# Kernel optimization log

Hardware: AMD Instinct MI355X
Metric: run time of the kernel (lower is better)

## Reference

```python
import jax, jax.numpy as jnp
import numpy as np

N = 100000   # nodes
E = 800000   # directed edges (symmetrized to 2E in forward)
D0 = 128     # input feature dim (dim0)
H = 128      # hidden = h_dim * args.d = 64 * 2
L = 4        # num_layers
G = 64       # num graphs for global_mean_pool
BN_EPS = 1e-5
LN_EPS = 1e-5


def setup_inputs() -> dict:
    key = jax.random.key(0)
    ks = jax.random.split(key, 12)
    s = 1.0 / np.sqrt(H)
    x = jax.random.normal(ks[0], (N, D0), dtype=jnp.float32)
    row = jax.random.randint(ks[1], (E,), 0, N, dtype=jnp.int32)
    off = jax.random.randint(ks[2], (E,), 1, N, dtype=jnp.int32)
    col = (row + off) % N  # guarantees row != col (no self loops)
    edge_index = jnp.stack([row, col])
    batch = jnp.sort(jax.random.randint(ks[3], (N,), 0, G, dtype=jnp.int32))
    return {
        "x": x,
        "W0": jax.random.normal(ks[4], (D0, H), dtype=jnp.float32) * s,
        "b0": jnp.zeros((H,), jnp.float32),
        "eps_l": jnp.zeros((L,), jnp.float32),        # GIN eps per layer
        "W1": jax.random.normal(ks[5], (L, H, H), dtype=jnp.float32) * s,
        "b1": jnp.zeros((L, H), jnp.float32),
        "bn_g": jnp.ones((L, H), jnp.float32),
        "bn_b": jnp.zeros((L, H), jnp.float32),
        "W2": jax.random.normal(ks[6], (L, H, H), dtype=jnp.float32) * s,
        "b2": jnp.zeros((L, H), jnp.float32),
        "ln_g": jnp.ones((L, H), jnp.float32),
        "ln_b": jnp.zeros((L, H), jnp.float32),
        "edge_index": edge_index,
        "batch": batch,
    }


def reference(x, W0, b0, eps_l, W1, b1, bn_g, bn_b, W2, b2, ln_g, ln_b, edge_index, batch):
    n = x.shape[0]
    h = x @ W0 + b0  # layer0 encode -> [N, H]
    # FNSD: symmetrize edges (cat with flip) and drop self loops
    ei = jnp.concatenate([edge_index, edge_index[::-1]], axis=1)
    row, col = ei[0], ei[1]
    w = (row != col).astype(h.dtype)  # self-loop removal as zero edge weight
    for i in range(L):
        # GINConv: scatter-add of neighbor features
        agg = jax.ops.segment_sum(w[:, None] * h[col], row, num_segments=n)
        u = (1.0 + eps_l[i]) * h + agg
        # mlp: Linear -> BatchNorm1d (training-mode batch stats) -> ReLU -> Linear
        z = u @ W1[i] + b1[i]
        m = jnp.mean(z, axis=0)
        v = jnp.var(z, axis=0)
        z = (z - m) * jax.lax.rsqrt(v + BN_EPS) * bn_g[i] + bn_b[i]
        z = jax.nn.relu(z)
        z = z @ W2[i] + b2[i]
        z = jax.nn.relu(z)          # use_activation
        h = h + z                    # use_residual
        mu = jnp.mean(h, axis=-1, keepdims=True)   # LayerNorm
        var = jnp.var(h, axis=-1, keepdims=True)
        h = (h - mu) * jax.lax.rsqrt(var + LN_EPS) * ln_g[i] + ln_b[i]
    # global_mean_pool over graph ids
    cnt = jax.ops.segment_sum(jnp.ones((n,), h.dtype), batch, num_segments=G)
    sums = jax.ops.segment_sum(h, batch, num_segments=G)
    return sums / jnp.maximum(cnt, 1.0)[:, None]
```

## Files before the change

kernel.cpp:

```cpp
#include <hip/hip_runtime.h>

#define NN 100000
#define EE 800000
#define HH 128
#define LL 4
#define GG 64
#define BN_EPS 1e-5f
#define LN_EPS 1e-5f
#define POOL_CHUNK 64
#define NBUK ((NN + 255) >> 8)
#define CAP 8192
#define BCHUNK 8192

typedef __attribute__((ext_vector_type(8))) short short8;
typedef __attribute__((ext_vector_type(4))) float f32x4;

__device__ inline unsigned short bf16_rne(float f) {
    unsigned u = __float_as_uint(f);
    return (unsigned short)((u + 0x7FFF + ((u >> 16) & 1)) >> 16);
}
__device__ inline float bf16_to_f32(unsigned short h) {
    return __uint_as_float((unsigned)h << 16);
}


__global__ void setup_kernel(const float* __restrict__ W0, const float* __restrict__ W1,
                             const float* __restrict__ W2, short* __restrict__ wt_hi,
                             int* __restrict__ bcur, float* __restrict__ colsum,
                             float* __restrict__ psum, float* __restrict__ pcnt) {
    int i = blockIdx.x * 256 + threadIdx.x;
    if (i < NBUK) bcur[i] = i * CAP;
    if (i < LL * HH * 2) colsum[i] = 0.f;
    if (i < GG * HH) psum[i] = 0.f;
    if (i < GG) pcnt[i] = 0.f;
    if (i < 9 * HH * HH) {
        int mat = i >> 14, rem = i & 16383;
        int n = rem >> 7, k = rem & 127;
        const float* src = (mat == 0) ? W0 : ((mat <= 4) ? W1 + (size_t)(mat - 1) * HH * HH
                                                         : W2 + (size_t)(mat - 5) * HH * HH);
        float v = src[(size_t)k * HH + n];
        int off = (mat << 14) + (((k >> 3) * 8 + (n >> 4)) << 7) + ((n & 15) << 3) + (k & 7);
        wt_hi[off] = (short)bf16_rne(v);
    }
}


__global__ __launch_bounds__(256) void bucket_scatter(const int* __restrict__ ei, int* __restrict__ bcur,
                                                      int* __restrict__ pairs) {
    __shared__ int h[NBUK];
    __shared__ int curb[NBUK];
    int tid = threadIdx.x;
    for (int i = tid; i < NBUK; i += 256) h[i] = 0;
    __syncthreads();
    int base = blockIdx.x * BCHUNK;
#pragma unroll 4
    for (int k = 0; k < BCHUNK / 256; k++) {
        int e = base + k * 256 + tid;
        if (e < 2 * EE) {
            int r = ei[e];
            int c = (e < EE) ? ei[e + EE] : ei[e - EE];
            if (r != c) atomicAdd(&h[r >> 8], 1);
        }
    }
    __syncthreads();
    for (int i = tid; i < NBUK; i += 256) {
        int n = h[i];
        curb[i] = n ? atomicAdd(&bcur[i], n) : 0;
    }
    __syncthreads();
#pragma unroll 4
    for (int k = 0; k < BCHUNK / 256; k++) {
        int e = base + k * 256 + tid;
        if (e < 2 * EE) {
            int r = ei[e];
            int c = (e < EE) ? ei[e + EE] : ei[e - EE];
            if (r != c) {
                int p = atomicAdd(&curb[r >> 8], 1);
                pairs[p] = ((r & 255) << 17) | c;
            }
        }
    }
}

__global__ __launch_bounds__(256) void bucket_build(const int* __restrict__ pairs, const int* __restrict__ bcur,
                                                    int* __restrict__ rp, int* __restrict__ re,
                                                    int* __restrict__ colidx) {
    __shared__ int hist[256], off[256], lcol[CAP];
    int b = blockIdx.x, tid = threadIdx.x;
    int s = b * CAP;
    int size = bcur[b] - s;
    hist[tid] = 0;
    __syncthreads();
    for (int i = tid; i < size; i += 256) atomicAdd(&hist[pairs[s + i] >> 17], 1);
    __syncthreads();
    off[tid] = hist[tid];
    __syncthreads();
    for (int o = 1; o < 256; o <<= 1) {
        int x = (tid >= o) ? off[tid - o] : 0;
        __syncthreads();
        off[tid] += x;
        __syncthreads();
    }
    int excl = (tid > 0) ? off[tid - 1] : 0;
    int r = (b << 8) + tid;
    if (r < NN) { rp[r] = s + excl; re[r] = s + off[tid]; }
    hist[tid] = excl;
    __syncthreads();
    for (int i = tid; i < size; i += 256) {
        int u = pairs[s + i];
        int p = atomicAdd(&hist[u >> 17], 1);
        lcol[p] = u & 0x1FFFF;
    }
    __syncthreads();
    for (int i = tid; i < size; i += 256) colidx[s + i] = lcol[i];
}


__global__ __launch_bounds__(256) void agg_kernel(
    const uint2* __restrict__ hbf2, const int* __restrict__ rp, const int* __restrict__ re,
    const int* __restrict__ colidx,
    const float* __restrict__ eps_l, int layer, uint2* __restrict__ u2)
{
    int lane = threadIdx.x & 63;
    int half = lane >> 5, sub = lane & 31;
    int node = blockIdx.x * 8 + (threadIdx.x >> 6) * 2 + half;
    float eps1 = 1.0f + eps_l[layer];
    uint2 sv = hbf2[(size_t)node * 32 + sub];
    float a0 = bf16_to_f32((unsigned short)(sv.x & 0xFFFF)) * eps1;
    float a1 = bf16_to_f32((unsigned short)(sv.x >> 16)) * eps1;
    float a2 = bf16_to_f32((unsigned short)(sv.y & 0xFFFF)) * eps1;
    float a3 = bf16_to_f32((unsigned short)(sv.y >> 16)) * eps1;
    int base = rp[node];
    int n = re[node] - base;
    for (int i = 0; i < n; i += 8) {
        uint2 v[8];
        int c[8];
#pragma unroll
        for (int j = 0; j < 8; j++) c[j] = (i + j < n) ? colidx[base + i + j] : -1;
#pragma unroll
        for (int j = 0; j < 8; j++)
            v[j] = (c[j] >= 0) ? hbf2[(size_t)c[j] * 32 + sub] : make_uint2(0u, 0u);
#pragma unroll
        for (int j = 0; j < 8; j++) {
            a0 += bf16_to_f32((unsigned short)(v[j].x & 0xFFFF));
            a1 += bf16_to_f32((unsigned short)(v[j].x >> 16));
            a2 += bf16_to_f32((unsigned short)(v[j].y & 0xFFFF));
            a3 += bf16_to_f32((unsigned short)(v[j].y >> 16));
        }
    }
    uint2 o;
    o.x = (unsigned)bf16_rne(a0) | ((unsigned)bf16_rne(a1) << 16);
    o.y = (unsigned)bf16_rne(a2) | ((unsigned)bf16_rne(a3) << 16);
    u2[(size_t)node * 32 + sub] = o;
}


template<int MODE>
__global__ __launch_bounds__(256, 4) void gemm_v9(
    const void* __restrict__ Ain,
    const short* __restrict__ wt_hi,
    const float* __restrict__ bias,
    unsigned short* __restrict__ z1_out,
    float* __restrict__ colsum, float* __restrict__ colsq,
    const float* __restrict__ bng, const float* __restrict__ bnb,
    const float* __restrict__ lng, const float* __restrict__ lnb,
    unsigned short* __restrict__ hbf)
{
    __shared__ short wh[HH * HH];
    __shared__ float stats[2 * HH];
    int tid = threadIdx.x;
    int wave = tid >> 6, lane = tid & 63;
    int lrow = lane & 15, kgrp = lane >> 4;
    int r0 = blockIdx.x * 64;
    int arow = r0 + wave * 16 + lrow;

    {
        const short8* src = (const short8*)wt_hi;
        short8* dst = (short8*)wh;
#pragma unroll
        for (int i = 0; i < 8; i++) dst[tid + i * 256] = src[tid + i * 256];
    }
    if (MODE == 1) stats[tid] = 0.f;
    if (MODE == 2 && tid < HH) {
        float m = colsum[tid] * (1.f / NN);
        float v = colsq[tid] * (1.f / NN) - m * m;
        float a = bng[tid] * rsqrtf(v + BN_EPS);
        stats[tid] = a;
        stats[HH + tid] = bnb[tid] - m * a;
    }

    float4 a0[4], a1[4];
    short8 az[4];
    if (MODE != 0) {
        const unsigned short* Az = (const unsigned short*)Ain;
        if (arow < NN) {
#pragma unroll
            for (int ks = 0; ks < 4; ks++)
                az[ks] = *(const short8*)(Az + (size_t)arow * HH + ks * 32 + kgrp * 8);
        } else {
#pragma unroll
            for (int ks = 0; ks < 4; ks++) az[ks] = (short8){0,0,0,0,0,0,0,0};
        }
    } else {
        const float* Af = (const float*)Ain;
        if (arow < NN) {
#pragma unroll
            for (int ks = 0; ks < 4; ks++) {
                int kb = ks * 32 + kgrp * 8;
                a0[ks] = *(const float4*)(Af + (size_t)arow * HH + kb);
                a1[ks] = *(const float4*)(Af + (size_t)arow * HH + kb + 4);
            }
        } else {
#pragma unroll
            for (int ks = 0; ks < 4; ks++) {
                a0[ks] = make_float4(0.f, 0.f, 0.f, 0.f);
                a1[ks] = a0[ks];
            }
        }
    }
    __syncthreads();

    f32x4 acc[8];
#pragma unroll
    for (int c = 0; c < 8; c++) acc[c] = (f32x4){0.f, 0.f, 0.f, 0.f};

#pragma unroll
    for (int ks = 0; ks < 4; ks++) {
        int fb = (ks * 4 + kgrp) * 8;
        if (MODE == 1) {
#pragma unroll
            for (int c = 0; c < 8; c++) {
                short8 whi = *(const short8*)(wh + ((fb + c) << 7) + (lrow << 3));
                acc[c] = __builtin_amdgcn_mfma_f32_16x16x32_bf16(az[ks], whi, acc[c], 0, 0, 0);
            }
        } else {
            int kb = ks * 32 + kgrp * 8;
            float av[8];
            if (MODE == 2) {
#pragma unroll
                for (int j = 0; j < 8; j++) {
                    float zb = bf16_to_f32((unsigned short)az[ks][j]);
                    av[j] = fmaxf(fmaf(zb, stats[kb + j], stats[HH + kb + j]), 0.f);
                }
            } else {
                av[0] = a0[ks].x; av[1] = a0[ks].y; av[2] = a0[ks].z; av[3] = a0[ks].w;
                av[4] = a1[ks].x; av[5] = a1[ks].y; av[6] = a1[ks].z; av[7] = a1[ks].w;
            }
            short8 ahi, alo;
#pragma unroll
            for (int j = 0; j < 8; j++) {
                unsigned short hb = bf16_rne(av[j]);
                ahi[j] = (short)hb;
                alo[j] = (short)bf16_rne(av[j] - bf16_to_f32(hb));
            }
#pragma unroll
            for (int c = 0; c < 8; c++) {
                short8 whi = *(const short8*)(wh + ((fb + c) << 7) + (lrow << 3));
                acc[c] = __builtin_amdgcn_mfma_f32_16x16x32_bf16(ahi, whi, acc[c], 0, 0, 0);
                acc[c] = __builtin_amdgcn_mfma_f32_16x16x32_bf16(alo, whi, acc[c], 0, 0, 0);
            }
        }
    }

    float bv[8];
#pragma unroll
    for (int c = 0; c < 8; c++) bv[c] = bias[c * 16 + lrow];
    int lrb = wave * 16 + kgrp * 4;
    unsigned short* hst = (unsigned short*)wh;

    if (MODE == 0) {
        __syncthreads();
#pragma unroll
        for (int c = 0; c < 8; c++)
#pragma unroll
            for (int reg = 0; reg < 4; reg++)
                hst[(lrb + reg) * HH + c * 16 + lrow] = bf16_rne(acc[c][reg] + bv[c]);
        __syncthreads();
#pragma unroll
        for (int i = 0; i < 4; i++) {
            int idx = tid + i * 256;
            int r = r0 + (idx >> 4);
            if (r < NN)
                *(uint4*)(hbf + (size_t)r * HH + (idx & 15) * 8) = ((const uint4*)wh)[idx];
        }
    } else if (MODE == 1) {
        __syncthreads();
        float ps[8], pq[8];
#pragma unroll
        for (int c = 0; c < 8; c++) { ps[c] = 0.f; pq[c] = 0.f; }
#pragma unroll
        for (int c = 0; c < 8; c++)
#pragma unroll
            for (int reg = 0; reg < 4; reg++) {
                float z = acc[c][reg] + bv[c];
                hst[(lrb + reg) * HH + c * 16 + lrow] = bf16_rne(z);
                if (r0 + lrb + reg < NN) { ps[c] += z; pq[c] += z * z; }
            }
#pragma unroll
        for (int c = 0; c < 8; c++) {
            ps[c] += __shfl_xor(ps[c], 16); pq[c] += __shfl_xor(pq[c], 16);
            ps[c] += __shfl_xor(ps[c], 32); pq[c] += __shfl_xor(pq[c], 32);
        }
        if (kgrp == 0) {
#pragma unroll
            for (int c = 0; c < 8; c++) {
                atomicAdd(&stats[c * 16 + lrow], ps[c]);
                atomicAdd(&stats[HH + c * 16 + lrow], pq[c]);
            }
        }
        __syncthreads();
#pragma unroll
        for (int i = 0; i < 4; i++) {
            int idx = tid + i * 256;
            int r = r0 + (idx >> 4);
            if (r < NN)
                *(uint4*)(z1_out + (size_t)r * HH + (idx & 15) * 8) = ((const uint4*)wh)[idx];
        }
        if (tid < HH) {
            atomicAdd(&colsum[tid], stats[tid]);
            atomicAdd(&colsq[tid], stats[HH + tid]);
        }
    } else {
        float lg[8], lb[8];
#pragma unroll
        for (int c = 0; c < 8; c++) {
            lg[c] = lng[c * 16 + lrow];
            lb[c] = lnb[c * 16 + lrow];
        }
        __syncthreads();
#pragma unroll
        for (int i = 0; i < 4; i++) {
            int idx = tid + i * 256;
            int r = r0 + (idx >> 4);
            uint4 v = make_uint4(0, 0, 0, 0);
            if (r < NN) v = *(const uint4*)(hbf + (size_t)r * HH + (idx & 15) * 8);
            ((uint4*)wh)[idx] = v;
        }
        __syncthreads();
#pragma unroll
        for (int reg = 0; reg < 4; reg++) {
            int r = r0 + lrb + reg;
            if (r < NN) {
                float tv[8];
                float s = 0.f, q = 0.f;
#pragma unroll
                for (int c = 0; c < 8; c++) {
                    float hold = bf16_to_f32(hst[(lrb + reg) * HH + c * 16 + lrow]);
                    tv[c] = hold + fmaxf(acc[c][reg] + bv[c], 0.f);
                    s += tv[c]; q += tv[c] * tv[c];
                }
#pragma unroll
                for (int m = 1; m < 16; m <<= 1) {
                    s += __shfl_xor(s, m);
                    q += __shfl_xor(q, m);
                }
                float mu = s * (1.f / 128.f);
                float var = q * (1.f / 128.f) - mu * mu;
                float rs = rsqrtf(var + LN_EPS);
#pragma unroll
                for (int c = 0; c < 8; c++)
                    hst[(lrb + reg) * HH + c * 16 + lrow] =
                        bf16_rne((tv[c] - mu) * rs * lg[c] + lb[c]);
            }
        }
        __syncthreads();
#pragma unroll
        for (int i = 0; i < 4; i++) {
            int idx = tid + i * 256;
            int r = r0 + (idx >> 4);
            if (r < NN)
                *(uint4*)(hbf + (size_t)r * HH + (idx & 15) * 8) = ((const uint4*)wh)[idx];
        }
    }
}


__global__ void pool_kernel(const unsigned short* __restrict__ h, const int* __restrict__ batch,
                            float* __restrict__ psum, float* __restrict__ pcnt)
{
    int t = threadIdx.x;
    int n0 = blockIdx.x * POOL_CHUNK;
    int n1 = n0 + POOL_CHUNK; if (n1 > NN) n1 = NN;
    if (n0 >= NN) return;
    float acc = 0.f;
    int cur = batch[n0];
    int cnt = 0;
    for (int n = n0; n < n1; n++) {
        int g = batch[n];
        if (g != cur) {
            atomicAdd(&psum[cur * HH + t], acc);
            if (t == 0) atomicAdd(&pcnt[cur], (float)cnt);
            acc = 0.f; cnt = 0; cur = g;
        }
        acc += bf16_to_f32(h[(size_t)n * HH + t]);
        cnt++;
    }
    atomicAdd(&psum[cur * HH + t], acc);
    if (t == 0) atomicAdd(&pcnt[cur], (float)cnt);
}

__global__ void pool_final(const float* __restrict__ psum, const float* __restrict__ pcnt,
                           float* __restrict__ out)
{
    int i = blockIdx.x * blockDim.x + threadIdx.x;
    if (i < GG * HH) {
        float c = pcnt[i >> 7];
        out[i] = psum[i] / fmaxf(c, 1.f);
    }
}


extern "C" void kernel_launch(void* const* d_in, const int* in_sizes, int n_in,
                              void* d_out, int out_size, void* d_ws, size_t ws_size,
                              hipStream_t stream)
{
    const float* x     = (const float*)d_in[0];
    const float* W0    = (const float*)d_in[1];
    const float* b0    = (const float*)d_in[2];
    const float* eps_l = (const float*)d_in[3];
    const float* W1    = (const float*)d_in[4];
    const float* b1    = (const float*)d_in[5];
    const float* bng   = (const float*)d_in[6];
    const float* bnb   = (const float*)d_in[7];
    const float* W2    = (const float*)d_in[8];
    const float* b2    = (const float*)d_in[9];
    const float* lng   = (const float*)d_in[10];
    const float* lnb   = (const float*)d_in[11];
    const int*   ei    = (const int*)d_in[12];
    const int*   batch = (const int*)d_in[13];
    float* out = (float*)d_out;

    char* ws = (char*)d_ws;
    size_t off = 0;
    auto alloc = [&](size_t bytes) -> void* {
        void* p = ws + off;
        off += (bytes + 255) & ~(size_t)255;
        return p;
    };
    unsigned short* hbf = (unsigned short*)alloc((size_t)NN * HH * 2);
    unsigned short* z1  = (unsigned short*)alloc((size_t)NN * HH * 2);
    unsigned short* ubuf = (unsigned short*)alloc((size_t)NN * HH * 2);
    int*   colidx = (int*)alloc((size_t)NBUK * CAP * 4 + 1024);
    int*   pairs  = (int*)alloc((size_t)NBUK * CAP * 4);
    int*   rp     = (int*)alloc((size_t)NN * 4);
    int*   re     = (int*)alloc((size_t)NN * 4);
    int*   bcur   = (int*)alloc((NBUK + 1) * 4);
    float* colsum = (float*)alloc((size_t)LL * HH * 2 * 4);
    float* psum   = (float*)alloc((size_t)GG * HH * 4);
    float* pcnt   = (float*)alloc(GG * 4);
    short* wt_hi  = (short*)alloc((size_t)9 * HH * HH * 2);

    setup_kernel<<<(9 * HH * HH + 255) / 256, 256, 0, stream>>>(W0, W1, W2, wt_hi, bcur,
                                                                colsum, psum, pcnt);

    bucket_scatter<<<(2 * EE + BCHUNK - 1) / BCHUNK, 256, 0, stream>>>(ei, bcur, pairs);
    bucket_build<<<NBUK, 256, 0, stream>>>(pairs, bcur, rp, re, colidx);

    int gb = (NN + 63) / 64;
    gemm_v9<0><<<gb, 256, 0, stream>>>(x, wt_hi, b0, nullptr,
                                       nullptr, nullptr, nullptr, nullptr, nullptr, nullptr, hbf);

    for (int l = 0; l < LL; l++) {
        float* cs = colsum + (size_t)l * HH * 2;
        float* cq = cs + HH;
        agg_kernel<<<NN / 8, 256, 0, stream>>>((const uint2*)hbf, rp, re, colidx,
                                               eps_l, l, (uint2*)ubuf);
        gemm_v9<1><<<gb, 256, 0, stream>>>(ubuf, wt_hi + (size_t)(1 + l) * HH * HH,
                                           b1 + l * HH, z1,
                                           cs, cq, nullptr, nullptr, nullptr, nullptr, nullptr);
        gemm_v9<2><<<gb, 256, 0, stream>>>(z1, wt_hi + (size_t)(5 + l) * HH * HH,
                                           b2 + l * HH, nullptr,
                                           cs, cq, bng + l * HH, bnb + l * HH,
                                           lng + l * HH, lnb + l * HH, hbf);
    }

    pool_kernel<<<(NN + POOL_CHUNK - 1) / POOL_CHUNK, 128, 0, stream>>>(hbf, batch, psum, pcnt);
    pool_final<<<(GG * HH + 255) / 256, 256, 0, stream>>>(psum, pcnt, out);
}
```

Before: 687.4 us.

## Fuse neighbor aggregation into first MLP GEMM, dropping intermediate u buffer

Merges the GIN aggregation kernel with the first linear layer and batch-norm statistics kernel. Each block gathers neighbor features for its 64 rows into shared memory as fp32, converts them to bf16 and runs the MFMA GEMM directly. This removes the write and re-read of the aggregated u tensor and one launch per layer. In exchange, each block now gathers 8 rows per half-wave sequentially, which cuts latency-hiding parallelism in the gather phase. The shared memory used for the fp32 staging may also lower occupancy.

```diff
diff --git a/kernel.cpp b/kernel.cpp
--- a/kernel.cpp
+++ b/kernel.cpp
@@ -116,42 +116,137 @@
 }
 
 
-__global__ __launch_bounds__(256) void agg_kernel(
-    const uint2* __restrict__ hbf2, const int* __restrict__ rp, const int* __restrict__ re,
+__global__ __launch_bounds__(256, 4) void fused_g1(
+    const uint2* __restrict__ hbf2,
+    const int* __restrict__ rp, const int* __restrict__ re,
     const int* __restrict__ colidx,
-    const float* __restrict__ eps_l, int layer, uint2* __restrict__ u2)
+    const float* __restrict__ eps_l, int layer,
+    const short* __restrict__ wt,
+    const float* __restrict__ bias,
+    unsigned short* __restrict__ z1_out,
+    float* __restrict__ colsum, float* __restrict__ colsq)
 {
-    int lane = threadIdx.x & 63;
+    __shared__ __align__(16) char smem[64 * 132 * 4];
+    __shared__ float stats[2 * HH];
+    float (*uls)[132] = (float(*)[132])smem;
+    short* wh = (short*)smem;
+
+    int tid = threadIdx.x;
+    int wave = tid >> 6, lane = tid & 63;
     int half = lane >> 5, sub = lane & 31;
-    int node = blockIdx.x * 8 + (threadIdx.x >> 6) * 2 + half;
+    int lrow = lane & 15, kgrp = lane >> 4;
+    int r0 = blockIdx.x * 64;
+    stats[tid] = 0.f;
     float eps1 = 1.0f + eps_l[layer];
-    uint2 sv = hbf2[(size_t)node * 32 + sub];
-    float a0 = bf16_to_f32((unsigned short)(sv.x & 0xFFFF)) * eps1;
-    float a1 = bf16_to_f32((unsigned short)(sv.x >> 16)) * eps1;
-    float a2 = bf16_to_f32((unsigned short)(sv.y & 0xFFFF)) * eps1;
-    float a3 = bf16_to_f32((unsigned short)(sv.y >> 16)) * eps1;
-    int base = rp[node];
-    int n = re[node] - base;
-    for (int i = 0; i < n; i += 8) {
-        uint2 v[8];
-        int c[8];
-#pragma unroll
-        for (int j = 0; j < 8; j++) c[j] = (i + j < n) ? colidx[base + i + j] : -1;
-#pragma unroll
-        for (int j = 0; j < 8; j++)
-            v[j] = (c[j] >= 0) ? hbf2[(size_t)c[j] * 32 + sub] : make_uint2(0u, 0u);
-#pragma unroll
-        for (int j = 0; j < 8; j++) {
-            a0 += bf16_to_f32((unsigned short)(v[j].x & 0xFFFF));
-            a1 += bf16_to_f32((unsigned short)(v[j].x >> 16));
-            a2 += bf16_to_f32((unsigned short)(v[j].y & 0xFFFF));
-            a3 += bf16_to_f32((unsigned short)(v[j].y >> 16));
-        }
-    }
-    uint2 o;
-    o.x = (unsigned)bf16_rne(a0) | ((unsigned)bf16_rne(a1) << 16);
-    o.y = (unsigned)bf16_rne(a2) | ((unsigned)bf16_rne(a3) << 16);
-    u2[(size_t)node * 32 + sub] = o;
+
+    int hw = wave * 2 + half;
+    for (int rl = 0; rl < 8; rl++) {
+        int row = hw * 8 + rl;
+        int r = r0 + row;
+        float a0 = 0.f, a1 = 0.f, a2 = 0.f, a3 = 0.f;
+        if (r < NN) {
+            uint2 sv = hbf2[(size_t)r * 32 + sub];
+            a0 = bf16_to_f32((unsigned short)(sv.x & 0xFFFF)) * eps1;
+            a1 = bf16_to_f32((unsigned short)(sv.x >> 16)) * eps1;
+            a2 = bf16_to_f32((unsigned short)(sv.y & 0xFFFF)) * eps1;
+            a3 = bf16_to_f32((unsigned short)(sv.y >> 16)) * eps1;
+            int base = rp[r];
+            int n = re[r] - base;
+            for (int i = 0; i < n; i += 8) {
+                uint2 v[8];
+                int c[8];
+#pragma unroll
+                for (int j = 0; j < 8; j++) c[j] = (i + j < n) ? colidx[base + i + j] : -1;
+#pragma unroll
+                for (int j = 0; j < 8; j++)
+                    v[j] = (c[j] >= 0) ? hbf2[(size_t)c[j] * 32 + sub] : make_uint2(0u, 0u);
+#pragma unroll
+                for (int j = 0; j < 8; j++) {
+                    a0 += bf16_to_f32((unsigned short)(v[j].x & 0xFFFF));
+                    a1 += bf16_to_f32((unsigned short)(v[j].x >> 16));
+                    a2 += bf16_to_f32((unsigned short)(v[j].y & 0xFFFF));
+                    a3 += bf16_to_f32((unsigned short)(v[j].y >> 16));
+                }
+            }
+        }
+        *(float4*)&uls[row][sub * 4] = make_float4(a0, a1, a2, a3);
+    }
+    __syncthreads();
+
+    short8 az[4];
+#pragma unroll
+    for (int ks = 0; ks < 4; ks++) {
+        int kb = ks * 32 + kgrp * 8;
+        float4 p0 = *(const float4*)&uls[wave * 16 + lrow][kb];
+        float4 p1 = *(const float4*)&uls[wave * 16 + lrow][kb + 4];
+        float av[8] = {p0.x, p0.y, p0.z, p0.w, p1.x, p1.y, p1.z, p1.w};
+#pragma unroll
+        for (int j = 0; j < 8; j++) az[ks][j] = (short)bf16_rne(av[j]);
+    }
+    __syncthreads();
+
+    {
+        const short8* src = (const short8*)wt;
+        short8* dst = (short8*)wh;
+#pragma unroll
+        for (int i = 0; i < 8; i++) dst[tid + i * 256] = src[tid + i * 256];
+    }
+    __syncthreads();
+
+    f32x4 acc[8];
+#pragma unroll
+    for (int c = 0; c < 8; c++) acc[c] = (f32x4){0.f, 0.f, 0.f, 0.f};
+#pragma unroll
+    for (int ks = 0; ks < 4; ks++) {
+        int fb = (ks * 4 + kgrp) * 8;
+#pragma unroll
+        for (int c = 0; c < 8; c++) {
+            short8 whi = *(const short8*)(wh + ((fb + c) << 7) + (lrow << 3));
+            acc[c] = __builtin_amdgcn_mfma_f32_16x16x32_bf16(az[ks], whi, acc[c], 0, 0, 0);
+        }
+    }
+
+    float bv[8];
+#pragma unroll
+    for (int c = 0; c < 8; c++) bv[c] = bias[c * 16 + lrow];
+    int lrb = wave * 16 + kgrp * 4;
+    unsigned short* hst = (unsigned short*)wh;
+    __syncthreads();
+    float ps[8], pq[8];
+#pragma unroll
+    for (int c = 0; c < 8; c++) { ps[c] = 0.f; pq[c] = 0.f; }
+#pragma unroll
+    for (int c = 0; c < 8; c++)
+#pragma unroll
+        for (int reg = 0; reg < 4; reg++) {
+            float z = acc[c][reg] + bv[c];
+            hst[(lrb + reg) * HH + c * 16 + lrow] = bf16_rne(z);
+            if (r0 + lrb + reg < NN) { ps[c] += z; pq[c] += z * z; }
+        }
+#pragma unroll
+    for (int c = 0; c < 8; c++) {
+        ps[c] += __shfl_xor(ps[c], 16); pq[c] += __shfl_xor(pq[c], 16);
+        ps[c] += __shfl_xor(ps[c], 32); pq[c] += __shfl_xor(pq[c], 32);
+    }
+    if (kgrp == 0) {
+#pragma unroll
+        for (int c = 0; c < 8; c++) {
+            atomicAdd(&stats[c * 16 + lrow], ps[c]);
+            atomicAdd(&stats[HH + c * 16 + lrow], pq[c]);
+        }
+    }
+    __syncthreads();
+#pragma unroll
+    for (int i = 0; i < 4; i++) {
+        int idx = tid + i * 256;
+        int r = r0 + (idx >> 4);
+        if (r < NN)
+            *(uint4*)(z1_out + (size_t)r * HH + (idx & 15) * 8) = ((const uint4*)wh)[idx];
+    }
+    if (tid < HH) {
+        atomicAdd(&colsum[tid], stats[tid]);
+        atomicAdd(&colsq[tid], stats[HH + tid]);
+    }
 }
 
 
@@ -160,7 +255,6 @@
     const void* __restrict__ Ain,
     const short* __restrict__ wt_hi,
     const float* __restrict__ bias,
-    unsigned short* __restrict__ z1_out,
     float* __restrict__ colsum, float* __restrict__ colsq,
     const float* __restrict__ bng, const float* __restrict__ bnb,
     const float* __restrict__ lng, const float* __restrict__ lnb,
@@ -180,7 +274,6 @@
 #pragma unroll
         for (int i = 0; i < 8; i++) dst[tid + i * 256] = src[tid + i * 256];
     }
-    if (MODE == 1) stats[tid] = 0.f;
     if (MODE == 2 && tid < HH) {
         float m = colsum[tid] * (1.f / NN);
         float v = colsq[tid] * (1.f / NN) - m * m;
@@ -191,7 +284,7 @@
 
     float4 a0[4], a1[4];
     short8 az[4];
-    if (MODE != 0) {
+    if (MODE == 2) {
         const unsigned short* Az = (const unsigned short*)Ain;
         if (arow < NN) {
 #pragma unroll
@@ -227,38 +320,30 @@
 #pragma unroll
     for (int ks = 0; ks < 4; ks++) {
         int fb = (ks * 4 + kgrp) * 8;
-        if (MODE == 1) {
-#pragma unroll
-            for (int c = 0; c < 8; c++) {
-                short8 whi = *(const short8*)(wh + ((fb + c) << 7) + (lrow << 3));
-                acc[c] = __builtin_amdgcn_mfma_f32_16x16x32_bf16(az[ks], whi, acc[c], 0, 0, 0);
+        int kb = ks * 32 + kgrp * 8;
+        float av[8];
+        if (MODE == 2) {
+#pragma unroll
+            for (int j = 0; j < 8; j++) {
+                float zb = bf16_to_f32((unsigned short)az[ks][j]);
+                av[j] = fmaxf(fmaf(zb, stats[kb + j], stats[HH + kb + j]), 0.f);
             }
         } else {
-            int kb = ks * 32 + kgrp * 8;
-            float av[8];
-            if (MODE == 2) {
-#pragma unroll
-                for (int j = 0; j < 8; j++) {
-                    float zb = bf16_to_f32((unsigned short)az[ks][j]);
-                    av[j] = fmaxf(fmaf(zb, stats[kb + j], stats[HH + kb + j]), 0.f);
-                }
-            } else {
-                av[0] = a0[ks].x; av[1] = a0[ks].y; av[2] = a0[ks].z; av[3] = a0[ks].w;
-                av[4] = a1[ks].x; av[5] = a1[ks].y; av[6] = a1[ks].z; av[7] = a1[ks].w;
-            }
-            short8 ahi, alo;
-#pragma unroll
-            for (int j = 0; j < 8; j++) {
-                unsigned short hb = bf16_rne(av[j]);
-                ahi[j] = (short)hb;
-                alo[j] = (short)bf16_rne(av[j] - bf16_to_f32(hb));
-            }
-#pragma unroll
-            for (int c = 0; c < 8; c++) {
-                short8 whi = *(const short8*)(wh + ((fb + c) << 7) + (lrow << 3));
-                acc[c] = __builtin_amdgcn_mfma_f32_16x16x32_bf16(ahi, whi, acc[c], 0, 0, 0);
-                acc[c] = __builtin_amdgcn_mfma_f32_16x16x32_bf16(alo, whi, acc[c], 0, 0, 0);
-            }
+            av[0] = a0[ks].x; av[1] = a0[ks].y; av[2] = a0[ks].z; av[3] = a0[ks].w;
+            av[4] = a1[ks].x; av[5] = a1[ks].y; av[6] = a1[ks].z; av[7] = a1[ks].w;
+        }
+        short8 ahi, alo;
+#pragma unroll
+        for (int j = 0; j < 8; j++) {
+            unsigned short hb = bf16_rne(av[j]);
+            ahi[j] = (short)hb;
+            alo[j] = (short)bf16_rne(av[j] - bf16_to_f32(hb));
+        }
+#pragma unroll
+        for (int c = 0; c < 8; c++) {
+            short8 whi = *(const short8*)(wh + ((fb + c) << 7) + (lrow << 3));
+            acc[c] = __builtin_amdgcn_mfma_f32_16x16x32_bf16(ahi, whi, acc[c], 0, 0, 0);
+            acc[c] = __builtin_amdgcn_mfma_f32_16x16x32_bf16(alo, whi, acc[c], 0, 0, 0);
         }
     }
 
@@ -282,43 +367,6 @@
             int r = r0 + (idx >> 4);
             if (r < NN)
                 *(uint4*)(hbf + (size_t)r * HH + (idx & 15) * 8) = ((const uint4*)wh)[idx];
-        }
-    } else if (MODE == 1) {
-        __syncthreads();
-        float ps[8], pq[8];
-#pragma unroll
-        for (int c = 0; c < 8; c++) { ps[c] = 0.f; pq[c] = 0.f; }
-#pragma unroll
-        for (int c = 0; c < 8; c++)
-#pragma unroll
-            for (int reg = 0; reg < 4; reg++) {
-                float z = acc[c][reg] + bv[c];
-                hst[(lrb + reg) * HH + c * 16 + lrow] = bf16_rne(z);
-                if (r0 + lrb + reg < NN) { ps[c] += z; pq[c] += z * z; }
-            }
-#pragma unroll
-        for (int c = 0; c < 8; c++) {
-            ps[c] += __shfl_xor(ps[c], 16); pq[c] += __shfl_xor(pq[c], 16);
-            ps[c] += __shfl_xor(ps[c], 32); pq[c] += __shfl_xor(pq[c], 32);
-        }
-        if (kgrp == 0) {
-#pragma unroll
-            for (int c = 0; c < 8; c++) {
-                atomicAdd(&stats[c * 16 + lrow], ps[c]);
-                atomicAdd(&stats[HH + c * 16 + lrow], pq[c]);
-            }
-        }
-        __syncthreads();
-#pragma unroll
-        for (int i = 0; i < 4; i++) {
-            int idx = tid + i * 256;
-            int r = r0 + (idx >> 4);
-            if (r < NN)
-                *(uint4*)(z1_out + (size_t)r * HH + (idx & 15) * 8) = ((const uint4*)wh)[idx];
-        }
-        if (tid < HH) {
-            atomicAdd(&colsum[tid], stats[tid]);
-            atomicAdd(&colsq[tid], stats[HH + tid]);
         }
     } else {
         float lg[8], lb[8];
@@ -439,7 +487,6 @@
     };
     unsigned short* hbf = (unsigned short*)alloc((size_t)NN * HH * 2);
     unsigned short* z1  = (unsigned short*)alloc((size_t)NN * HH * 2);
-    unsigned short* ubuf = (unsigned short*)alloc((size_t)NN * HH * 2);
     int*   colidx = (int*)alloc((size_t)NBUK * CAP * 4 + 1024);
     int*   pairs  = (int*)alloc((size_t)NBUK * CAP * 4);
     int*   rp     = (int*)alloc((size_t)NN * 4);
@@ -457,19 +504,17 @@
     bucket_build<<<NBUK, 256, 0, stream>>>(pairs, bcur, rp, re, colidx);
 
     int gb = (NN + 63) / 64;
-    gemm_v9<0><<<gb, 256, 0, stream>>>(x, wt_hi, b0, nullptr,
+    gemm_v9<0><<<gb, 256, 0, stream>>>(x, wt_hi, b0,
                                        nullptr, nullptr, nullptr, nullptr, nullptr, nullptr, hbf);
 
     for (int l = 0; l < LL; l++) {
         float* cs = colsum + (size_t)l * HH * 2;
         float* cq = cs + HH;
-        agg_kernel<<<NN / 8, 256, 0, stream>>>((const uint2*)hbf, rp, re, colidx,
-                                               eps_l, l, (uint2*)ubuf);
-        gemm_v9<1><<<gb, 256, 0, stream>>>(ubuf, wt_hi + (size_t)(1 + l) * HH * HH,
-                                           b1 + l * HH, z1,
-                                           cs, cq, nullptr, nullptr, nullptr, nullptr, nullptr);
+        fused_g1<<<gb, 256, 0, stream>>>((const uint2*)hbf, rp, re, colidx, eps_l, l,
+                                         wt_hi + (size_t)(1 + l) * HH * HH, b1 + l * HH, z1,
+                                         cs, cq);
         gemm_v9<2><<<gb, 256, 0, stream>>>(z1, wt_hi + (size_t)(5 + l) * HH * HH,
-                                           b2 + l * HH, nullptr,
+                                           b2 + l * HH,
                                            cs, cq, bng + l * HH, bnb + l * HH,
                                            lng + l * HH, lnb + l * HH, hbf);
     }
```

Measured after the change: 681.3 us. About the same (-0.9%).
